# Kernel tuning notes

Measured on AMD Instinct MI355X. Metric: run time of the kernel, lower is better.

The kernel has to match this reference:

```python
import jax, jax.numpy as jnp
import numpy as np

D_MODEL = 2048
H_Q = 32
H_KV = 8
D_HEAD = D_MODEL // H_Q   # 64
G = H_Q // H_KV           # 4 query heads per kv head
B, S = 2, 2048


def setup_inputs() -> dict:
    key = jax.random.key(0)
    ks = jax.random.split(key, 7)
    s = 0.02  # weight init scale
    return {
        "q": jax.random.normal(ks[0], (B, S, D_MODEL), jnp.float32),
        "k": jax.random.normal(ks[1], (B, S, D_MODEL), jnp.float32),
        "v": jax.random.normal(ks[2], (B, S, D_MODEL), jnp.float32),
        "Wq": jax.random.normal(ks[3], (D_MODEL, D_MODEL), jnp.float32) * s,
        "Wk": jax.random.normal(ks[4], (D_MODEL, H_KV * D_HEAD), jnp.float32) * s,
        "Wv": jax.random.normal(ks[5], (D_MODEL, H_KV * D_HEAD), jnp.float32) * s,
        "Wo": jax.random.normal(ks[6], (D_MODEL, D_MODEL), jnp.float32) * s,
    }


def reference(q, k, v, Wq, Wk, Wv, Wo):
    # Projections (torch Linear with bias=False: x @ W^T; here W stored as [in,out])
    b, s, _ = q.shape
    # repeat_interleave(k, G, -2) maps kv head j -> query heads j*G..j*G+G-1,
    # i.e. query head h uses kv head h // G. Reshape q heads as (H_KV, G)
    # kv-head-major instead of materializing expanded K/V.
    qh = (q @ Wq).reshape(b, s, H_KV, G, D_HEAD)
    kh = (k @ Wk).reshape(b, s, H_KV, D_HEAD)
    vh = (v @ Wv).reshape(b, s, H_KV, D_HEAD)
    scale = 1.0 / jnp.sqrt(jnp.asarray(D_HEAD, qh.dtype))
    # scores: [B, H_KV, G, Sq, Sk]
    scores = jnp.einsum('bqhgd,bkhd->bhgqk', qh, kh) * scale
    attn = jax.nn.softmax(scores, axis=-1)
    # context: [B, Sq, H_KV, G, D_HEAD]
    ctx = jnp.einsum('bhgqk,bkhd->bqhgd', attn, vh)
    out = ctx.reshape(b, s, D_MODEL) @ Wo
    return out
```

## Files before the change

kernel.cpp:

```cpp
#include <hip/hip_runtime.h>
#include <stdint.h>


typedef __attribute__((ext_vector_type(8))) short short8;
typedef __attribute__((ext_vector_type(4))) float float4v;
typedef __attribute__((ext_vector_type(4))) unsigned short ushort4v;
typedef __attribute__((ext_vector_type(4))) unsigned int uint4v;

__device__ __forceinline__ unsigned short f2bf(float f) {
  union { float f; unsigned int u; } v; v.f = f;
  unsigned int r = v.u + 0x7fffu + ((v.u >> 16) & 1u);
  return (unsigned short)(r >> 16);
}
__device__ __forceinline__ unsigned int fbits(float f) {
  union { float f; unsigned int u; } v; v.f = f; return v.u;
}
__device__ __forceinline__ unsigned int pack_bf16_trunc(float lo, float hi) {
  return __builtin_amdgcn_perm(fbits(hi), fbits(lo), 0x07060302u);
}

__device__ __forceinline__ void gl2lds16(const unsigned short* g, unsigned short* l) {
  __builtin_amdgcn_global_load_lds(
      (const __attribute__((address_space(1))) void*)g,
      (__attribute__((address_space(3))) void*)l, 16, 0, 0);
}

__global__ void prep(const float* __restrict__ q, const float* __restrict__ k,
                     const float* __restrict__ v,
                     const float* __restrict__ Wq, const float* __restrict__ Wk,
                     const float* __restrict__ Wv,
                     unsigned short* __restrict__ qb, unsigned short* __restrict__ kb,
                     unsigned short* __restrict__ vb,
                     unsigned short* __restrict__ WTq, unsigned short* __restrict__ WTk,
                     unsigned short* __restrict__ WTv)
{
  __shared__ unsigned short t[32][33];
  const int z = blockIdx.z;
  if (z >= 3) {
    const float* in  = (z == 3) ? q : (z == 4) ? k : v;
    unsigned short* out = (z == 3) ? qb : (z == 4) ? kb : vb;
    const int tid = threadIdx.y * 32 + threadIdx.x;
    const int bid = blockIdx.y * 64 + blockIdx.x;
    for (int i = bid * 256 + tid; i < 2097152; i += 4096 * 256) {
      const float4v a = *(const float4v*)(in + (size_t)i * 4);
      *(ushort4v*)(out + (size_t)i * 4) = (ushort4v){f2bf(a.x), f2bf(a.y), f2bf(a.z), f2bf(a.w)};
    }
    return;
  }
  const float* in; unsigned short* out; int R, C;
  if (z == 0)      { in = Wq; out = WTq; R = 2048; C = 2048; }
  else if (z == 1) { in = Wk; out = WTk; R = 2048; C = 512; }
  else             { in = Wv; out = WTv; R = 2048; C = 512; }
  const int x0 = blockIdx.x * 32, y0 = blockIdx.y * 32;
  if (x0 >= C) return;
  const int tx = threadIdx.x, ty = threadIdx.y;
#pragma unroll
  for (int i = 0; i < 4; ++i) {
    const int r = y0 + ty + i * 8, c = x0 + tx;
    t[ty + i * 8][tx] = f2bf(in[(size_t)r * C + c]);
  }
  __syncthreads();
#pragma unroll
  for (int i = 0; i < 4; ++i)
    out[(size_t)(x0 + ty + i * 8) * R + y0 + tx] = t[tx][ty + i * 8];
}

__global__ void transpose_bf16(const float* __restrict__ inp, unsigned short* __restrict__ out,
                               int R, int C) {
  __shared__ unsigned short t[32][33];
  const int x0 = blockIdx.x * 32, y0 = blockIdx.y * 32;
  const int tx = threadIdx.x, ty = threadIdx.y;
#pragma unroll
  for (int i = 0; i < 4; ++i) {
    const int r = y0 + ty + i * 8, c = x0 + tx;
    t[ty + i * 8][tx] = f2bf(inp[(size_t)r * C + c]);
  }
  __syncthreads();
#pragma unroll
  for (int i = 0; i < 4; ++i)
    out[(size_t)(x0 + ty + i * 8) * R + y0 + tx] = t[tx][ty + i * 8];
}

template<int TN, bool C_BF16>
__device__ void gemm_body(const unsigned short* __restrict__ A,
                          const unsigned short* __restrict__ Bt,
                          void* __restrict__ C, int N, int K, float cscale,
                          int bx, int by)
{
  constexpr int NT = TN / 32;
  constexpr int BI = TN / 64;
  __shared__ unsigned short As[128][32];
  __shared__ unsigned short Bs[TN][32];

  const int tid  = threadIdx.x;
  const int wave = tid >> 6;
  const int lane = tid & 63;
  const int quad = lane >> 4;
  const int l15  = lane & 15;
  const int wm   = (wave >> 1) * 64;
  const int wn   = (wave & 1) * (TN / 2);
  const int m0   = by * 128;
  const int n0   = bx * TN;

  const int srow = lane >> 2;
  const int skof = (lane & 3) * 8;

  float4v acc[4][NT];
#pragma unroll
  for (int i = 0; i < 4; ++i)
#pragma unroll
    for (int j = 0; j < NT; ++j) acc[i][j] = (float4v)0.0f;

  for (int k0 = 0; k0 < K; k0 += 32) {
    __syncthreads();
#pragma unroll
    for (int i = 0; i < 2; ++i) {
      const int row = wave * 32 + i * 16 + srow;
      gl2lds16(A + (size_t)(m0 + row) * K + k0 + skof, &As[wave * 32 + i * 16][0]);
    }
#pragma unroll
    for (int i = 0; i < BI; ++i) {
      const int row = wave * (TN / 4) + i * 16 + srow;
      gl2lds16(Bt + (size_t)(n0 + row) * K + k0 + skof, &Bs[wave * (TN / 4) + i * 16][0]);
    }
    __syncthreads();

    short8 af[4], bf[NT];
#pragma unroll
    for (int mt = 0; mt < 4; ++mt)  af[mt] = *(const short8*)&As[wm + mt * 16 + l15][quad * 8];
#pragma unroll
    for (int nt = 0; nt < NT; ++nt) bf[nt] = *(const short8*)&Bs[wn + nt * 16 + l15][quad * 8];
#pragma unroll
    for (int mt = 0; mt < 4; ++mt)
#pragma unroll
      for (int nt = 0; nt < NT; ++nt)
        acc[mt][nt] = __builtin_amdgcn_mfma_f32_16x16x32_bf16(af[mt], bf[nt], acc[mt][nt], 0, 0, 0);
  }

#pragma unroll
  for (int mt = 0; mt < 4; ++mt)
#pragma unroll
    for (int nt = 0; nt < NT; ++nt) {
      const int row = m0 + wm + mt * 16 + quad * 4;
      const int col = n0 + wn + nt * 16 + l15;
#pragma unroll
      for (int r = 0; r < 4; ++r) {
        const float val = acc[mt][nt][r] * cscale;
        if (C_BF16) ((unsigned short*)C)[(size_t)(row + r) * N + col] = f2bf(val);
        else        ((float*)C)[(size_t)(row + r) * N + col] = val;
      }
    }
}

template<int TN, bool C_BF16>
__global__ __launch_bounds__(256, 2)
void gemm_bt(const unsigned short* __restrict__ A, const unsigned short* __restrict__ Bt,
             void* __restrict__ C, int N, int K, float cscale)
{
  gemm_body<TN, C_BF16>(A, Bt, C, N, K, cscale, blockIdx.x, blockIdx.y);
}

__global__ __launch_bounds__(256, 2)
void gemm_kv(const unsigned short* __restrict__ kb, const unsigned short* __restrict__ WTk,
             unsigned short* __restrict__ Kp,
             const unsigned short* __restrict__ WTv, const unsigned short* __restrict__ vb,
             unsigned short* __restrict__ VpT)
{
  const int id = blockIdx.x;
  if (id < 256) gemm_body<64, true>(kb, WTk, Kp, 512, 2048, 1.0f, id & 7, id >> 3);
  else          gemm_body<64, true>(WTv, vb, VpT, 4096, 2048, 1.0f, (id - 256) & 63, (id - 256) >> 6);
}

__global__ __launch_bounds__(256, 4)
void attn_flash(const unsigned short* __restrict__ Qp,
                const unsigned short* __restrict__ Kp,
                const unsigned short* __restrict__ VpT,
                unsigned short* __restrict__ Ctx)
{
  __shared__ unsigned short Ks[2][64 * 64];
  __shared__ unsigned short VTs[2][64 * 64];

  const int tid  = threadIdx.x;
  const int wave = tid >> 6;
  const int lane = tid & 63;
  const int quad = lane >> 4;
  const int l15  = lane & 15;

  const int head = blockIdx.y;
  const int b    = head >> 5;
  const int hq   = head & 31;
  const int hkv  = hq >> 2;
  const size_t qrow = (size_t)(b * 2048 + blockIdx.x * 128 + wave * 32);

  short8 qf[2][2];
#pragma unroll
  for (int mt = 0; mt < 2; ++mt)
#pragma unroll
    for (int kc = 0; kc < 2; ++kc)
      qf[mt][kc] = *(const short8*)&Qp[(qrow + mt * 16 + l15) * 2048 + hq * 64 + kc * 32 + quad * 8];

  float4v oa[2][4];
  float4v lacc[2];
#pragma unroll
  for (int mt = 0; mt < 2; ++mt) {
    lacc[mt] = (float4v)0.0f;
#pragma unroll
    for (int dt = 0; dt < 4; ++dt) oa[mt][dt] = (float4v)0.0f;
  }
  short8 ones;
#pragma unroll
  for (int i = 0; i < 8; ++i) ones[i] = (short)0x3F80;

  auto stage = [&](int j, int bu) {
#pragma unroll
    for (int i = 0; i < 2; ++i) {
      const int s  = i * 256 + wave * 64 + lane;
      const int r  = s >> 3;
      const int lc = (s & 7) ^ (r & 7);
      const int rk = ((r >> 4) & 1) * 32 + ((r >> 2) & 3) * 8 + (r >> 5) * 4 + (r & 3);
      gl2lds16(Kp + (size_t)(b * 2048 + j * 64 + rk) * 512 + hkv * 64 + lc * 8,
               &Ks[bu][i * 2048 + wave * 512]);
      gl2lds16(VpT + (size_t)(hkv * 64 + r) * 4096 + b * 2048 + j * 64 + lc * 8,
               &VTs[bu][i * 2048 + wave * 512]);
    }
  };

  stage(0, 0);
  __syncthreads();

  for (int j = 0; j < 32; ++j) {
    const int bu = j & 1;
    if (j < 31) stage(j + 1, bu ^ 1);

    short8 kf[4][2];
#pragma unroll
    for (int nt = 0; nt < 4; ++nt) {
      const int krow = nt * 16 + l15;
      kf[nt][0] = *(const short8*)&Ks[bu][krow * 64 + ((quad ^ (l15 & 7)) * 8)];
      kf[nt][1] = *(const short8*)&Ks[bu][krow * 64 + (((4 + quad) ^ (l15 & 7)) * 8)];
    }

    __builtin_amdgcn_s_setprio(1);

    unsigned int w[2][4][2];
#pragma unroll
    for (int mt = 0; mt < 2; ++mt) {
#pragma unroll
      for (int nt = 0; nt < 4; ++nt) {
        float4v sa = (float4v)0.0f;
        sa = __builtin_amdgcn_mfma_f32_16x16x32_bf16(kf[nt][0], qf[mt][0], sa, 0, 0, 0);
        sa = __builtin_amdgcn_mfma_f32_16x16x32_bf16(kf[nt][1], qf[mt][1], sa, 0, 0, 0);
        const float e0 = __builtin_amdgcn_exp2f(sa[0]);
        const float e1 = __builtin_amdgcn_exp2f(sa[1]);
        const float e2 = __builtin_amdgcn_exp2f(sa[2]);
        const float e3 = __builtin_amdgcn_exp2f(sa[3]);
        w[mt][nt][0] = pack_bf16_trunc(e0, e1);
        w[mt][nt][1] = pack_bf16_trunc(e2, e3);
      }
    }

#pragma unroll
    for (int kc = 0; kc < 2; ++kc) {
      union { uint4v u; short8 s; } p0u, p1u;
      p0u.u = (uint4v){w[0][kc][0], w[0][kc][1], w[0][kc + 2][0], w[0][kc + 2][1]};
      p1u.u = (uint4v){w[1][kc][0], w[1][kc][1], w[1][kc + 2][0], w[1][kc + 2][1]};
      const short8 pf0 = p0u.s;
      const short8 pf1 = p1u.s;
#pragma unroll
      for (int dt = 0; dt < 4; ++dt) {
        const int vrow = dt * 16 + l15;
        const short8 vf = *(const short8*)&VTs[bu][vrow * 64 + (((kc * 4 + quad) ^ (l15 & 7)) * 8)];
        oa[0][dt] = __builtin_amdgcn_mfma_f32_16x16x32_bf16(pf0, vf, oa[0][dt], 0, 0, 0);
        oa[1][dt] = __builtin_amdgcn_mfma_f32_16x16x32_bf16(pf1, vf, oa[1][dt], 0, 0, 0);
      }
      lacc[0] = __builtin_amdgcn_mfma_f32_16x16x32_bf16(pf0, ones, lacc[0], 0, 0, 0);
      lacc[1] = __builtin_amdgcn_mfma_f32_16x16x32_bf16(pf1, ones, lacc[1], 0, 0, 0);
    }

    __builtin_amdgcn_s_setprio(0);
    __syncthreads();
  }

#pragma unroll
  for (int mt = 0; mt < 2; ++mt)
#pragma unroll
    for (int r = 0; r < 4; ++r) {
      const float inv = 1.0f / lacc[mt][r];
#pragma unroll
      for (int dt = 0; dt < 4; ++dt)
        Ctx[(qrow + mt * 16 + quad * 4 + r) * 2048 + hq * 64 + dt * 16 + l15] =
            f2bf(oa[mt][dt][r] * inv);
    }
}

extern "C" void kernel_launch(void* const* d_in, const int* in_sizes, int n_in,
                              void* d_out, int out_size, void* d_ws, size_t ws_size,
                              hipStream_t stream)
{
  const float* q  = (const float*)d_in[0];
  const float* k  = (const float*)d_in[1];
  const float* v  = (const float*)d_in[2];
  const float* Wq = (const float*)d_in[3];
  const float* Wk = (const float*)d_in[4];
  const float* Wv = (const float*)d_in[5];
  const float* Wo = (const float*)d_in[6];
  float* out = (float*)d_out;

  unsigned short* ws  = (unsigned short*)d_ws;
  unsigned short* qb  = ws;
  unsigned short* kb  = qb  + (size_t)8388608;
  unsigned short* vb  = kb  + (size_t)8388608;
  unsigned short* WT  = vb  + (size_t)8388608;
  unsigned short* Qp  = WT  + (size_t)4194304;
  unsigned short* Kp  = Qp  + (size_t)8388608;
  unsigned short* VpT = Kp  + (size_t)2097152;
  unsigned short* Ctx = qb;
  unsigned short* WTk = Qp;
  unsigned short* WTv = Qp + (size_t)1048576;

  const dim3 blk(256);
  const dim3 tblk(32, 8);
  const float SM_SCALE = 0.125f * 1.44269504089f;

  prep<<<dim3(64, 64, 6), tblk, 0, stream>>>(q, k, v, Wq, Wk, Wv,
                                             qb, kb, vb, WT, WTk, WTv);

  gemm_kv<<<dim3(512), blk, 0, stream>>>(kb, WTk, Kp, WTv, vb, VpT);

  gemm_bt<128, true><<<dim3(16, 32), blk, 0, stream>>>(qb, WT, Qp, 2048, 2048, SM_SCALE);

  transpose_bf16<<<dim3(64, 64), tblk, 0, stream>>>(Wo, WT, 2048, 2048);

  attn_flash<<<dim3(16, 64), blk, 0, stream>>>(Qp, Kp, VpT, Ctx);

  gemm_bt<128, false><<<dim3(16, 32), blk, 0, stream>>>(Ctx, WT, out, 2048, 2048, 1.0f);
}
```

Measured before the change: 382.7 us.

## Merge Q/K/V projection GEMMs, swizzle block order, software-pipeline attention QK/exp with PV

```diff
diff --git a/kernel.cpp b/kernel.cpp
--- a/kernel.cpp
+++ b/kernel.cpp
@@ -152,32 +152,46 @@
     }
 }
 
-template<int TN, bool C_BF16>
 __global__ __launch_bounds__(256, 2)
-void gemm_bt(const unsigned short* __restrict__ A, const unsigned short* __restrict__ Bt,
-             void* __restrict__ C, int N, int K, float cscale)
-{
-  gemm_body<TN, C_BF16>(A, Bt, C, N, K, cscale, blockIdx.x, blockIdx.y);
-}
-
+void gemm_mid(const unsigned short* __restrict__ qb, const unsigned short* __restrict__ WTq,
+              unsigned short* __restrict__ Qp,
+              const unsigned short* __restrict__ kb, const unsigned short* __restrict__ WTk,
+              unsigned short* __restrict__ Kp,
+              const unsigned short* __restrict__ WTv, const unsigned short* __restrict__ vb,
+              unsigned short* __restrict__ VpT, float sm_scale)
+{
+  const int id = blockIdx.x;
+  if (id < 512) {
+    const int s = (id & 7) * 64 + (id >> 3);
+    gemm_body<128, true>(qb, WTq, Qp, 2048, 2048, sm_scale, s & 15, s >> 4);
+  } else if (id < 768) {
+    const int t = id - 512;
+    const int s = (t & 7) * 32 + (t >> 3);
+    gemm_body<64, true>(kb, WTk, Kp, 512, 2048, 1.0f, s & 7, s >> 3);
+  } else {
+    const int t = id - 768;
+    const int s = (t & 7) * 32 + (t >> 3);
+    gemm_body<64, true>(WTv, vb, VpT, 4096, 2048, 1.0f, s & 63, s >> 6);
+  }
+}
+
+template<int TN, bool C_BF16, int GX>
 __global__ __launch_bounds__(256, 2)
-void gemm_kv(const unsigned short* __restrict__ kb, const unsigned short* __restrict__ WTk,
-             unsigned short* __restrict__ Kp,
-             const unsigned short* __restrict__ WTv, const unsigned short* __restrict__ vb,
-             unsigned short* __restrict__ VpT)
-{
-  const int id = blockIdx.x;
-  if (id < 256) gemm_body<64, true>(kb, WTk, Kp, 512, 2048, 1.0f, id & 7, id >> 3);
-  else          gemm_body<64, true>(WTv, vb, VpT, 4096, 2048, 1.0f, (id - 256) & 63, (id - 256) >> 6);
-}
-
-__global__ __launch_bounds__(256, 4)
+void gemm_swz(const unsigned short* __restrict__ A, const unsigned short* __restrict__ Bt,
+              void* __restrict__ C, int N, int K, float cscale)
+{
+  const int chunk = gridDim.x >> 3;
+  const int s = (blockIdx.x & 7) * chunk + (blockIdx.x >> 3);
+  gemm_body<TN, C_BF16>(A, Bt, C, N, K, cscale, s % GX, s / GX);
+}
+
+__global__ __launch_bounds__(256, 2)
 void attn_flash(const unsigned short* __restrict__ Qp,
                 const unsigned short* __restrict__ Kp,
                 const unsigned short* __restrict__ VpT,
                 unsigned short* __restrict__ Ctx)
 {
-  __shared__ unsigned short Ks[2][64 * 64];
+  __shared__ unsigned short Ks[3][64 * 64];
   __shared__ unsigned short VTs[2][64 * 64];
 
   const int tid  = threadIdx.x;
@@ -211,7 +225,7 @@
 #pragma unroll
   for (int i = 0; i < 8; ++i) ones[i] = (short)0x3F80;
 
-  auto stage = [&](int j, int bu) {
+  auto stageK = [&](int j, int bu) {
 #pragma unroll
     for (int i = 0; i < 2; ++i) {
       const int s  = i * 256 + wave * 64 + lane;
@@ -220,65 +234,133 @@
       const int rk = ((r >> 4) & 1) * 32 + ((r >> 2) & 3) * 8 + (r >> 5) * 4 + (r & 3);
       gl2lds16(Kp + (size_t)(b * 2048 + j * 64 + rk) * 512 + hkv * 64 + lc * 8,
                &Ks[bu][i * 2048 + wave * 512]);
+    }
+  };
+  auto stageV = [&](int j, int bu) {
+#pragma unroll
+    for (int i = 0; i < 2; ++i) {
+      const int s  = i * 256 + wave * 64 + lane;
+      const int r  = s >> 3;
+      const int lc = (s & 7) ^ (r & 7);
       gl2lds16(VpT + (size_t)(hkv * 64 + r) * 4096 + b * 2048 + j * 64 + lc * 8,
                &VTs[bu][i * 2048 + wave * 512]);
     }
   };
 
-  stage(0, 0);
-  __syncthreads();
-
-  for (int j = 0; j < 32; ++j) {
-    const int bu = j & 1;
-    if (j < 31) stage(j + 1, bu ^ 1);
-
+  auto qkexp = [&](int kb3, unsigned int (&w)[2][4][2]) {
     short8 kf[4][2];
 #pragma unroll
     for (int nt = 0; nt < 4; ++nt) {
       const int krow = nt * 16 + l15;
-      kf[nt][0] = *(const short8*)&Ks[bu][krow * 64 + ((quad ^ (l15 & 7)) * 8)];
-      kf[nt][1] = *(const short8*)&Ks[bu][krow * 64 + (((4 + quad) ^ (l15 & 7)) * 8)];
-    }
-
-    __builtin_amdgcn_s_setprio(1);
-
-    unsigned int w[2][4][2];
-#pragma unroll
-    for (int mt = 0; mt < 2; ++mt) {
+      kf[nt][0] = *(const short8*)&Ks[kb3][krow * 64 + ((quad ^ (l15 & 7)) * 8)];
+      kf[nt][1] = *(const short8*)&Ks[kb3][krow * 64 + (((4 + quad) ^ (l15 & 7)) * 8)];
+    }
+#pragma unroll
+    for (int mt = 0; mt < 2; ++mt)
 #pragma unroll
       for (int nt = 0; nt < 4; ++nt) {
         float4v sa = (float4v)0.0f;
         sa = __builtin_amdgcn_mfma_f32_16x16x32_bf16(kf[nt][0], qf[mt][0], sa, 0, 0, 0);
         sa = __builtin_amdgcn_mfma_f32_16x16x32_bf16(kf[nt][1], qf[mt][1], sa, 0, 0, 0);
-        const float e0 = __builtin_amdgcn_exp2f(sa[0]);
-        const float e1 = __builtin_amdgcn_exp2f(sa[1]);
-        const float e2 = __builtin_amdgcn_exp2f(sa[2]);
-        const float e3 = __builtin_amdgcn_exp2f(sa[3]);
-        w[mt][nt][0] = pack_bf16_trunc(e0, e1);
-        w[mt][nt][1] = pack_bf16_trunc(e2, e3);
+        w[mt][nt][0] = pack_bf16_trunc(__builtin_amdgcn_exp2f(sa[0]), __builtin_amdgcn_exp2f(sa[1]));
+        w[mt][nt][1] = pack_bf16_trunc(__builtin_amdgcn_exp2f(sa[2]), __builtin_amdgcn_exp2f(sa[3]));
       }
-    }
-
-#pragma unroll
-    for (int kc = 0; kc < 2; ++kc) {
+  };
+
+  auto body = [&](int j, int dstK, int rdK,
+                  unsigned int (&wcur)[2][4][2], unsigned int (&wnext)[2][4][2]) {
+    if (j < 30) stageK(j + 2, dstK);
+    if (j < 31) stageV(j + 1, (j + 1) & 1);
+    const int vb2 = j & 1;
+
+    __builtin_amdgcn_s_setprio(1);
+    float4v sa[2][4];
+    if (j < 31) {
+      short8 kf[4][2];
+#pragma unroll
+      for (int nt = 0; nt < 4; ++nt) {
+        const int krow = nt * 16 + l15;
+        kf[nt][0] = *(const short8*)&Ks[rdK][krow * 64 + ((quad ^ (l15 & 7)) * 8)];
+        kf[nt][1] = *(const short8*)&Ks[rdK][krow * 64 + (((4 + quad) ^ (l15 & 7)) * 8)];
+      }
+#pragma unroll
+      for (int mt = 0; mt < 2; ++mt)
+#pragma unroll
+        for (int nt = 0; nt < 4; ++nt) {
+          sa[mt][nt] = (float4v)0.0f;
+          sa[mt][nt] = __builtin_amdgcn_mfma_f32_16x16x32_bf16(kf[nt][0], qf[mt][0], sa[mt][nt], 0, 0, 0);
+          sa[mt][nt] = __builtin_amdgcn_mfma_f32_16x16x32_bf16(kf[nt][1], qf[mt][1], sa[mt][nt], 0, 0, 0);
+        }
+    }
+
+    {
       union { uint4v u; short8 s; } p0u, p1u;
-      p0u.u = (uint4v){w[0][kc][0], w[0][kc][1], w[0][kc + 2][0], w[0][kc + 2][1]};
-      p1u.u = (uint4v){w[1][kc][0], w[1][kc][1], w[1][kc + 2][0], w[1][kc + 2][1]};
-      const short8 pf0 = p0u.s;
-      const short8 pf1 = p1u.s;
+      p0u.u = (uint4v){wcur[0][0][0], wcur[0][0][1], wcur[0][2][0], wcur[0][2][1]};
+      p1u.u = (uint4v){wcur[1][0][0], wcur[1][0][1], wcur[1][2][0], wcur[1][2][1]};
 #pragma unroll
       for (int dt = 0; dt < 4; ++dt) {
         const int vrow = dt * 16 + l15;
-        const short8 vf = *(const short8*)&VTs[bu][vrow * 64 + (((kc * 4 + quad) ^ (l15 & 7)) * 8)];
-        oa[0][dt] = __builtin_amdgcn_mfma_f32_16x16x32_bf16(pf0, vf, oa[0][dt], 0, 0, 0);
-        oa[1][dt] = __builtin_amdgcn_mfma_f32_16x16x32_bf16(pf1, vf, oa[1][dt], 0, 0, 0);
+        const short8 vf = *(const short8*)&VTs[vb2][vrow * 64 + ((quad ^ (l15 & 7)) * 8)];
+        oa[0][dt] = __builtin_amdgcn_mfma_f32_16x16x32_bf16(p0u.s, vf, oa[0][dt], 0, 0, 0);
+        oa[1][dt] = __builtin_amdgcn_mfma_f32_16x16x32_bf16(p1u.s, vf, oa[1][dt], 0, 0, 0);
       }
-      lacc[0] = __builtin_amdgcn_mfma_f32_16x16x32_bf16(pf0, ones, lacc[0], 0, 0, 0);
-      lacc[1] = __builtin_amdgcn_mfma_f32_16x16x32_bf16(pf1, ones, lacc[1], 0, 0, 0);
-    }
-
+      lacc[0] = __builtin_amdgcn_mfma_f32_16x16x32_bf16(p0u.s, ones, lacc[0], 0, 0, 0);
+      lacc[1] = __builtin_amdgcn_mfma_f32_16x16x32_bf16(p1u.s, ones, lacc[1], 0, 0, 0);
+    }
+
+    if (j < 31) {
+#pragma unroll
+      for (int mt = 0; mt < 2; ++mt)
+#pragma unroll
+        for (int nt = 0; nt < 2; ++nt) {
+          wnext[mt][nt][0] = pack_bf16_trunc(__builtin_amdgcn_exp2f(sa[mt][nt][0]),
+                                             __builtin_amdgcn_exp2f(sa[mt][nt][1]));
+          wnext[mt][nt][1] = pack_bf16_trunc(__builtin_amdgcn_exp2f(sa[mt][nt][2]),
+                                             __builtin_amdgcn_exp2f(sa[mt][nt][3]));
+        }
+    }
+
+    {
+      union { uint4v u; short8 s; } p0u, p1u;
+      p0u.u = (uint4v){wcur[0][1][0], wcur[0][1][1], wcur[0][3][0], wcur[0][3][1]};
+      p1u.u = (uint4v){wcur[1][1][0], wcur[1][1][1], wcur[1][3][0], wcur[1][3][1]};
+#pragma unroll
+      for (int dt = 0; dt < 4; ++dt) {
+        const int vrow = dt * 16 + l15;
+        const short8 vf = *(const short8*)&VTs[vb2][vrow * 64 + (((4 + quad) ^ (l15 & 7)) * 8)];
+        oa[0][dt] = __builtin_amdgcn_mfma_f32_16x16x32_bf16(p0u.s, vf, oa[0][dt], 0, 0, 0);
+        oa[1][dt] = __builtin_amdgcn_mfma_f32_16x16x32_bf16(p1u.s, vf, oa[1][dt], 0, 0, 0);
+      }
+      lacc[0] = __builtin_amdgcn_mfma_f32_16x16x32_bf16(p0u.s, ones, lacc[0], 0, 0, 0);
+      lacc[1] = __builtin_amdgcn_mfma_f32_16x16x32_bf16(p1u.s, ones, lacc[1], 0, 0, 0);
+    }
+
+    if (j < 31) {
+#pragma unroll
+      for (int mt = 0; mt < 2; ++mt)
+#pragma unroll
+        for (int nt = 2; nt < 4; ++nt) {
+          wnext[mt][nt][0] = pack_bf16_trunc(__builtin_amdgcn_exp2f(sa[mt][nt][0]),
+                                             __builtin_amdgcn_exp2f(sa[mt][nt][1]));
+          wnext[mt][nt][1] = pack_bf16_trunc(__builtin_amdgcn_exp2f(sa[mt][nt][2]),
+                                             __builtin_amdgcn_exp2f(sa[mt][nt][3]));
+        }
+    }
     __builtin_amdgcn_s_setprio(0);
     __syncthreads();
+  };
+
+  stageK(0, 0); stageV(0, 0); stageK(1, 1);
+  __syncthreads();
+
+  unsigned int wA[2][4][2], wB[2][4][2];
+  qkexp(0, wA);
+
+  int bA = 0, bB = 1, bC = 2;
+  for (int j = 0; j < 32; j += 2) {
+    body(j,     bC, bB, wA, wB);
+    body(j + 1, bA, bC, wB, wA);
+    const int t = bA; bA = bC; bC = bB; bB = t;
   }
 
 #pragma unroll
@@ -315,8 +397,8 @@
   unsigned short* Kp  = Qp  + (size_t)8388608;
   unsigned short* VpT = Kp  + (size_t)2097152;
   unsigned short* Ctx = qb;
-  unsigned short* WTk = Qp;
-  unsigned short* WTv = Qp + (size_t)1048576;
+  unsigned short* WTk = (unsigned short*)d_out;
+  unsigned short* WTv = (unsigned short*)d_out + 1048576;
 
   const dim3 blk(256);
   const dim3 tblk(32, 8);
@@ -325,13 +407,11 @@
   prep<<<dim3(64, 64, 6), tblk, 0, stream>>>(q, k, v, Wq, Wk, Wv,
                                              qb, kb, vb, WT, WTk, WTv);
 
-  gemm_kv<<<dim3(512), blk, 0, stream>>>(kb, WTk, Kp, WTv, vb, VpT);
-
-  gemm_bt<128, true><<<dim3(16, 32), blk, 0, stream>>>(qb, WT, Qp, 2048, 2048, SM_SCALE);
+  gemm_mid<<<dim3(1024), blk, 0, stream>>>(qb, WT, Qp, kb, WTk, Kp, WTv, vb, VpT, SM_SCALE);
 
   transpose_bf16<<<dim3(64, 64), tblk, 0, stream>>>(Wo, WT, 2048, 2048);
 
   attn_flash<<<dim3(16, 64), blk, 0, stream>>>(Qp, Kp, VpT, Ctx);
 
-  gemm_bt<128, false><<<dim3(16, 32), blk, 0, stream>>>(Ctx, WT, out, 2048, 2048, 1.0f);
-}
+  gemm_swz<128, false, 16><<<dim3(512), blk, 0, stream>>>(Ctx, WT, out, 2048, 2048, 1.0f);
+}
```

Measured after the change: 362.4 us. 5.3% less time.
